# Performance work log

Hardware: AMD Instinct MI355X
Metric: run time of the kernel (lower is better)

Reference implementation:

```python
import jax, jax.numpy as jnp
import numpy as np

REL_CONTEXT = 0.2  # default forward arg

def setup_inputs() -> dict:
    key = jax.random.key(0)
    ks = jax.random.split(key, 8)
    B, M, D = 4096, 2, 2048
    return {
        "x": jax.random.normal(ks[0], (B, M, D), jnp.float32),
        "sub_type_ids": jax.random.randint(ks[1], (B, M), 0, M),
        "modal_weights": jnp.ones((M,), jnp.float32),
        "emb_table": jax.random.normal(ks[2], (M, D), jnp.float32),
        "Wt": jax.random.normal(ks[3], (D, D), jnp.float32) * (1.0 / np.sqrt(D)),
        "bt": jax.random.normal(ks[4], (D,), jnp.float32) * 0.01,
        "Wrc": jax.random.normal(ks[5], (1, D), jnp.float32) * (1.0 / np.sqrt(D)),
        "brc": jax.random.normal(ks[6], (1,), jnp.float32) * 0.01,
    }

def reference(x, sub_type_ids, modal_weights, emb_table, Wt, bt, Wrc, brc):
    B = x.shape[0]
    D = emb_table.shape[1]
    x = x.reshape(B, -1, D)  # [B, M, D]
    # relational gate: Linear(D->1) on a constant vector filled with 0.2 -> scalar
    rc = jnp.full((D,), REL_CONTEXT, dtype=x.dtype)
    zeta = jax.nn.sigmoid(rc @ Wrc.T + brc)  # [1]
    sub = emb_table[sub_type_ids]  # [B, M, D] embedding lookup
    # fused: per-modality Linear + ReLU (replaces the B*M python loop)
    t = jax.nn.relu(jnp.einsum('bmd,ed->bme', x + sub, Wt) + bt)  # [B, M, D]
    h = modal_weights[None, :, None] * t * zeta[0]
    # dropout is identity in eval mode; final ReLU as in the original
    return jax.nn.relu(h)
```

## Files before the change

### kernel.cpp

```cpp
#include <hip/hip_runtime.h>
#include <hip/hip_bf16.h>
#include <math.h>

#define MROWS 8192
#define KDIM  2048
#define NDIM  2048

#define BM 256
#define BN 128
#define BK 64

typedef short  v8s __attribute__((ext_vector_type(8)));
typedef float  v4f __attribute__((ext_vector_type(4)));

#define A_OFF   0ull
#define W_OFF   ((unsigned long long)MROWS * KDIM * 2ull)
#define MWZ_OFF (W_OFF + (unsigned long long)NDIM * KDIM * 2ull)

__device__ inline unsigned short f2bf(float f) {
    __hip_bfloat16 h = __float2bfloat16(f);
    return *reinterpret_cast<unsigned short*>(&h);
}

__global__ __launch_bounds__(256) void prep_kernel(
    const float* __restrict__ x, const int* __restrict__ ids,
    const float* __restrict__ mw, const float* __restrict__ emb,
    const float* __restrict__ Wrc, const float* __restrict__ brc,
    const float* __restrict__ Wt,
    unsigned short* __restrict__ Abf, unsigned short* __restrict__ Wbf,
    float* __restrict__ mwz)
{
    const int tid = threadIdx.x;

    if (blockIdx.x == 0) {
        __shared__ float red[256];
        float s = 0.f;
        for (int d = tid; d < KDIM; d += 256) s += Wrc[d];
        red[tid] = s;
        __syncthreads();
        for (int off = 128; off > 0; off >>= 1) {
            if (tid < off) red[tid] += red[tid + off];
            __syncthreads();
        }
        if (tid == 0) {
            float zeta = 1.0f / (1.0f + expf(-(0.2f * red[0] + brc[0])));
            mwz[0] = mw[0] * zeta;
            mwz[1] = mw[1] * zeta;
        }
    }

    const int groupsA = MROWS * KDIM / 8;
    for (int g = blockIdx.x * 256 + tid; g < groupsA; g += gridDim.x * 256) {
        const int row = g >> 8;
        const int off = (g & 255) << 3;
        const int st  = ids[row];
        const float4* xp = (const float4*)(x   + (size_t)row * KDIM + off);
        const float4* ep = (const float4*)(emb + (size_t)st  * KDIM + off);
        float4 x0 = xp[0], x1 = xp[1];
        float4 e0 = ep[0], e1 = ep[1];
        v8s o;
        o[0] = (short)f2bf(x0.x + e0.x);
        o[1] = (short)f2bf(x0.y + e0.y);
        o[2] = (short)f2bf(x0.z + e0.z);
        o[3] = (short)f2bf(x0.w + e0.w);
        o[4] = (short)f2bf(x1.x + e1.x);
        o[5] = (short)f2bf(x1.y + e1.y);
        o[6] = (short)f2bf(x1.z + e1.z);
        o[7] = (short)f2bf(x1.w + e1.w);
        *(v8s*)(Abf + (size_t)g * 8) = o;
    }

    const int groupsW = NDIM * KDIM / 8;
    for (int g = blockIdx.x * 256 + tid; g < groupsW; g += gridDim.x * 256) {
        const float4* wp = (const float4*)(Wt + (size_t)g * 8);
        float4 w0 = wp[0], w1 = wp[1];
        v8s o;
        o[0] = (short)f2bf(w0.x); o[1] = (short)f2bf(w0.y);
        o[2] = (short)f2bf(w0.z); o[3] = (short)f2bf(w0.w);
        o[4] = (short)f2bf(w1.x); o[5] = (short)f2bf(w1.y);
        o[6] = (short)f2bf(w1.z); o[7] = (short)f2bf(w1.w);
        *(v8s*)(Wbf + (size_t)g * 8) = o;
    }
}

__global__ __launch_bounds__(256, 2) void gemm_kernel(
    const unsigned short* __restrict__ Abf,
    const unsigned short* __restrict__ Wbf,
    const float* __restrict__ bt,
    const float* __restrict__ mwz,
    float* __restrict__ out)
{
    __shared__ __align__(16) unsigned short lA[BM * BK];
    __shared__ __align__(16) unsigned short lB[BN * BK];

    const int tid  = threadIdx.x;
    const int lane = tid & 63;
    const int wave = tid >> 6;
    const int wr   = wave & 1;
    const int wc   = wave >> 1;
    const int quad = lane >> 4;
    const int mcol = lane & 15;

    const int br = blockIdx.x;
    const int bc = blockIdx.y;

    v4f acc[8][4];
    const v4f vzero = {0.f, 0.f, 0.f, 0.f};
    #pragma unroll
    for (int i = 0; i < 8; i++)
        #pragma unroll
        for (int j = 0; j < 4; j++) acc[i][j] = vzero;

    const unsigned short* gA = Abf + (size_t)(br * BM) * KDIM;
    const unsigned short* gB = Wbf + (size_t)(bc * BN) * KDIM;

    for (int kt = 0; kt < KDIM; kt += BK) {
        #pragma unroll
        for (int q = 0; q < 8; q++) {
            const int f   = q * 256 + tid;
            const int row = f >> 3;
            const int ch  = (f & 7) ^ (row & 7);
            const unsigned short* ga = gA + (size_t)row * KDIM + kt + ch * 8;
            __builtin_amdgcn_global_load_lds(
                (const __attribute__((address_space(1))) void*)ga,
                (__attribute__((address_space(3))) void*)(&lA[(size_t)f * 8]),
                16, 0, 0);
        }
        #pragma unroll
        for (int q = 0; q < 4; q++) {
            const int f   = q * 256 + tid;
            const int row = f >> 3;
            const int ch  = (f & 7) ^ (row & 7);
            const unsigned short* gb = gB + (size_t)row * KDIM + kt + ch * 8;
            __builtin_amdgcn_global_load_lds(
                (const __attribute__((address_space(1))) void*)gb,
                (__attribute__((address_space(3))) void*)(&lB[(size_t)f * 8]),
                16, 0, 0);
        }
        __syncthreads();

        #pragma unroll
        for (int ks = 0; ks < BK; ks += 32) {
            v8s af[8], bf_[4];
            #pragma unroll
            for (int i = 0; i < 8; i++) {
                const int row = wr * 128 + i * 16 + mcol;
                const int cc  = (ks >> 3) + quad;
                const int c   = cc ^ (row & 7);
                af[i] = *(const v8s*)(&lA[row * BK + c * 8]);
            }
            #pragma unroll
            for (int j = 0; j < 4; j++) {
                const int col = wc * 64 + j * 16 + mcol;
                const int cc  = (ks >> 3) + quad;
                const int c   = cc ^ (col & 7);
                bf_[j] = *(const v8s*)(&lB[col * BK + c * 8]);
            }
            #pragma unroll
            for (int i = 0; i < 8; i++)
                #pragma unroll
                for (int j = 0; j < 4; j++)
                    acc[i][j] = __builtin_amdgcn_mfma_f32_16x16x32_bf16(
                        bf_[j], af[i], acc[i][j], 0, 0, 0);
        }
        __syncthreads();
    }

    const float mz = mwz[mcol & 1];
    #pragma unroll
    for (int j = 0; j < 4; j++) {
        const int ncol = bc * BN + wc * 64 + j * 16 + quad * 4;
        const float4 b4 = *(const float4*)(bt + ncol);
        #pragma unroll
        for (int i = 0; i < 8; i++) {
            const int row = br * BM + wr * 128 + i * 16 + mcol;
            float4 o;
            o.x = fmaxf(mz * fmaxf(acc[i][j][0] + b4.x, 0.0f), 0.0f);
            o.y = fmaxf(mz * fmaxf(acc[i][j][1] + b4.y, 0.0f), 0.0f);
            o.z = fmaxf(mz * fmaxf(acc[i][j][2] + b4.z, 0.0f), 0.0f);
            o.w = fmaxf(mz * fmaxf(acc[i][j][3] + b4.w, 0.0f), 0.0f);
            *(float4*)(out + (size_t)row * NDIM + ncol) = o;
        }
    }
}

extern "C" void kernel_launch(void* const* d_in, const int* in_sizes, int n_in,
                              void* d_out, int out_size, void* d_ws, size_t ws_size,
                              hipStream_t stream) {
    const float* x    = (const float*)d_in[0];
    const int*   ids  = (const int*)  d_in[1];
    const float* mw   = (const float*)d_in[2];
    const float* emb  = (const float*)d_in[3];
    const float* Wt   = (const float*)d_in[4];
    const float* bt   = (const float*)d_in[5];
    const float* Wrc  = (const float*)d_in[6];
    const float* brc  = (const float*)d_in[7];
    float* out = (float*)d_out;

    char* ws = (char*)d_ws;
    unsigned short* Abf = (unsigned short*)(ws + A_OFF);
    unsigned short* Wbf = (unsigned short*)(ws + W_OFF);
    float* mwz          = (float*)(ws + MWZ_OFF);

    prep_kernel<<<2048, 256, 0, stream>>>(x, ids, mw, emb, Wrc, brc, Wt,
                                          Abf, Wbf, mwz);

    dim3 grid(MROWS / BM, NDIM / BN);
    gemm_kernel<<<grid, 256, 0, stream>>>(Abf, Wbf, bt, mwz, out);
}
```

Before: 200.4 us.

## Double-buffer LDS tiles in GEMM with halved K-tile to overlap loads

Replaces the single-buffer GEMM main loop with a two-stage LDS ping-pong. The next K-tile is issued via global_load_lds while MFMAs run on the current one, and the loop drops to one barrier per iteration. BK is halved to 32 so both buffers fit in the same LDS budget, and the swizzle is reworked for 4 chunks per row. In exchange it runs twice as many iterations and barriers, and relies on the barrier to order the async LDS writes.

```diff
diff --git a/kernel.cpp b/kernel.cpp
--- a/kernel.cpp
+++ b/kernel.cpp
@@ -8,7 +8,7 @@
 
 #define BM 256
 #define BN 128
-#define BK 64
+#define BK 32
 
 typedef short  v8s __attribute__((ext_vector_type(8)));
 typedef float  v4f __attribute__((ext_vector_type(4)));
@@ -90,8 +90,8 @@
     const float* __restrict__ mwz,
     float* __restrict__ out)
 {
-    __shared__ __align__(16) unsigned short lA[BM * BK];
-    __shared__ __align__(16) unsigned short lB[BN * BK];
+    __shared__ __align__(16) unsigned short lA[2][BM * BK];
+    __shared__ __align__(16) unsigned short lB[2][BN * BK];
 
     const int tid  = threadIdx.x;
     const int lane = tid & 63;
@@ -114,57 +114,65 @@
     const unsigned short* gA = Abf + (size_t)(br * BM) * KDIM;
     const unsigned short* gB = Wbf + (size_t)(bc * BN) * KDIM;
 
-    for (int kt = 0; kt < KDIM; kt += BK) {
-        #pragma unroll
-        for (int q = 0; q < 8; q++) {
-            const int f   = q * 256 + tid;
-            const int row = f >> 3;
-            const int ch  = (f & 7) ^ (row & 7);
-            const unsigned short* ga = gA + (size_t)row * KDIM + kt + ch * 8;
-            __builtin_amdgcn_global_load_lds(
-                (const __attribute__((address_space(1))) void*)ga,
-                (__attribute__((address_space(3))) void*)(&lA[(size_t)f * 8]),
-                16, 0, 0);
-        }
-        #pragma unroll
-        for (int q = 0; q < 4; q++) {
-            const int f   = q * 256 + tid;
-            const int row = f >> 3;
-            const int ch  = (f & 7) ^ (row & 7);
-            const unsigned short* gb = gB + (size_t)row * KDIM + kt + ch * 8;
-            __builtin_amdgcn_global_load_lds(
-                (const __attribute__((address_space(1))) void*)gb,
-                (__attribute__((address_space(3))) void*)(&lB[(size_t)f * 8]),
-                16, 0, 0);
-        }
+    #define STAGE(KT, BUF)                                                     \
+        {                                                                      \
+            const int kt_ = (KT);                                              \
+            _Pragma("unroll")                                                  \
+            for (int q = 0; q < 4; q++) {                                      \
+                const int f   = q * 256 + tid;                                 \
+                const int row = f >> 2;                                        \
+                const int ch  = (f & 3) ^ (row & 3);                           \
+                const unsigned short* ga = gA + (size_t)row * KDIM + kt_ + ch * 8; \
+                __builtin_amdgcn_global_load_lds(                              \
+                    (const __attribute__((address_space(1))) void*)ga,         \
+                    (__attribute__((address_space(3))) void*)(&lA[BUF][(size_t)f * 8]), \
+                    16, 0, 0);                                                 \
+            }                                                                  \
+            _Pragma("unroll")                                                  \
+            for (int q = 0; q < 2; q++) {                                      \
+                const int f   = q * 256 + tid;                                 \
+                const int row = f >> 2;                                        \
+                const int ch  = (f & 3) ^ (row & 3);                           \
+                const unsigned short* gb = gB + (size_t)row * KDIM + kt_ + ch * 8; \
+                __builtin_amdgcn_global_load_lds(                              \
+                    (const __attribute__((address_space(1))) void*)gb,         \
+                    (__attribute__((address_space(3))) void*)(&lB[BUF][(size_t)f * 8]), \
+                    16, 0, 0);                                                 \
+            }                                                                  \
+        }
+
+    STAGE(0, 0);
+
+    const int NITER = KDIM / BK;
+    for (int it = 0; it < NITER; it++) {
+        const int cur = it & 1;
+        const int nxt = cur ^ 1;
+
         __syncthreads();
 
-        #pragma unroll
-        for (int ks = 0; ks < BK; ks += 32) {
-            v8s af[8], bf_[4];
+        if (it + 1 < NITER) STAGE((it + 1) * BK, nxt);
+
+        v8s af[8], bf_[4];
+        #pragma unroll
+        for (int i = 0; i < 8; i++) {
+            const int row = wr * 128 + i * 16 + mcol;
+            const int c   = quad ^ (row & 3);
+            af[i] = *(const v8s*)(&lA[cur][row * BK + c * 8]);
+        }
+        #pragma unroll
+        for (int j = 0; j < 4; j++) {
+            const int col = wc * 64 + j * 16 + mcol;
+            const int c   = quad ^ (col & 3);
+            bf_[j] = *(const v8s*)(&lB[cur][col * BK + c * 8]);
+        }
+        #pragma unroll
+        for (int i = 0; i < 8; i++)
             #pragma unroll
-            for (int i = 0; i < 8; i++) {
-                const int row = wr * 128 + i * 16 + mcol;
-                const int cc  = (ks >> 3) + quad;
-                const int c   = cc ^ (row & 7);
-                af[i] = *(const v8s*)(&lA[row * BK + c * 8]);
-            }
-            #pragma unroll
-            for (int j = 0; j < 4; j++) {
-                const int col = wc * 64 + j * 16 + mcol;
-                const int cc  = (ks >> 3) + quad;
-                const int c   = cc ^ (col & 7);
-                bf_[j] = *(const v8s*)(&lB[col * BK + c * 8]);
-            }
-            #pragma unroll
-            for (int i = 0; i < 8; i++)
-                #pragma unroll
-                for (int j = 0; j < 4; j++)
-                    acc[i][j] = __builtin_amdgcn_mfma_f32_16x16x32_bf16(
-                        bf_[j], af[i], acc[i][j], 0, 0, 0);
-        }
-        __syncthreads();
-    }
+            for (int j = 0; j < 4; j++)
+                acc[i][j] = __builtin_amdgcn_mfma_f32_16x16x32_bf16(
+                    bf_[j], af[i], acc[i][j], 0, 0, 0);
+    }
+    #undef STAGE
 
     const float mz = mwz[mcol & 1];
     #pragma unroll
```

New measurement: 229.0 us. +14.2%, slower.
